# Kernel optimization log

Hardware: AMD Instinct MI355X
Metric: run time of the kernel (lower is better)

The kernel has to match this reference:

```python
import jax, jax.numpy as jnp
import numpy as np

DIM = 768
HEADS = 12
HEAD_DIM = DIM // HEADS
SCALE = HEAD_DIM ** (-0.5)


def setup_inputs() -> dict:
    key = jax.random.key(0)
    k1, k2, k3, k4 = jax.random.split(key, 4)
    B, N = 2, 48 * 48
    x = jax.random.normal(k1, (B, N, DIM), dtype=jnp.float32)
    qkv_w = jax.random.normal(k2, (3 * DIM, DIM), dtype=jnp.float32) * (DIM ** -0.5)
    proj_w = jax.random.normal(k3, (DIM, DIM), dtype=jnp.float32) * (DIM ** -0.5)
    proj_b = jax.random.normal(k4, (DIM,), dtype=jnp.float32) * 0.02
    return {"x": x, "H": 48, "W": 48, "qkv_w": qkv_w, "proj_w": proj_w, "proj_b": proj_b}


def reference(x, H, W, qkv_w, proj_w, proj_b):
    B, N, C = x.shape
    h, d = HEADS, HEAD_DIM
    # qkv linear (no bias): [B,N,3C], then split into per-head q,k,v [B,h,N,d]
    qkv = jnp.einsum('bnc,fc->bnf', x, qkv_w)
    qkv = qkv.reshape(B, N, 3, h, d).transpose(2, 0, 3, 1, 4)
    q, k, v = qkv[0], qkv[1], qkv[2]
    attn = jnp.einsum('bhnd,bhmd->bhnm', q, k) * SCALE  # [B,h,N,N]
    attn = jax.nn.softmax(attn, axis=-1)
    out = jnp.einsum('bhnm,bhmd->bhnd', attn, v)  # [B,h,N,d]
    out = out.transpose(0, 2, 1, 3).reshape(B, N, C)
    out = jnp.einsum('bnc,fc->bnf', out, proj_w) + proj_b
    return out
```

## Files before the change

kernel.cpp:

```cpp
#include <hip/hip_runtime.h>

#define B_    2
#define N_    2304
#define C_    768
#define HEADS 12
#define D_    64
#define F3    2304
#define M_    (B_*N_)
#define SPLITS 2
#define KSPAN (N_/SPLITS)
#define QSCALE 0.18033688011112042f

typedef __attribute__((ext_vector_type(8)))  short bfrag;
typedef __attribute__((ext_vector_type(4)))  float ffrag;
typedef __attribute__((ext_vector_type(16))) float ffrag16;
typedef __attribute__((ext_vector_type(4)))  unsigned ufrag;

__device__ __forceinline__ short f2bf(float f) {
    unsigned u = __float_as_uint(f);
    u += 0x7fff + ((u >> 16) & 1);
    return (short)(u >> 16);
}

__device__ __forceinline__ void gl2lds16(const void* g, void* l) {
    __builtin_amdgcn_global_load_lds(
        (const __attribute__((address_space(1))) void*)g,
        (__attribute__((address_space(3))) void*)l, 16, 0, 0);
}

__device__ __forceinline__ unsigned pktrunc(float a, float b) {
    return __builtin_amdgcn_perm(__float_as_uint(a), __float_as_uint(b),
                                 0x03020706u);
}

__global__ __launch_bounds__(256) void cast_all(const float* __restrict__ x,
                                                const float* __restrict__ qw,
                                                const float* __restrict__ pw,
                                                short* __restrict__ dst) {
    const int nx4 = (M_*C_)/4, nq4 = (F3*C_)/4, np4 = (C_*C_)/4;
    int i = blockIdx.x * 256 + threadIdx.x;
    if (i >= nx4 + nq4 + np4) return;
    const float* src; int off;
    if (i < nx4)            { src = x;  off = i; }
    else if (i < nx4 + nq4) { src = qw; off = i - nx4; }
    else                    { src = pw; off = i - nx4 - nq4; }
    float4 v = ((const float4*)src)[off];
    short4 o;
    o.x = f2bf(v.x); o.y = f2bf(v.y); o.z = f2bf(v.z); o.w = f2bf(v.w);
    ((short4*)dst)[i] = o;
}

__global__ __launch_bounds__(256) void qkv_gemm(const short* __restrict__ xb,
                                                const short* __restrict__ wb,
                                                short* __restrict__ Qb,
                                                short* __restrict__ Kb,
                                                short* __restrict__ Vtb) {
    __shared__ short As[128*64];
    __shared__ short Bs[128*64];
    const int t = threadIdx.x;
    const int w = t >> 6, lane = t & 63;
    const int quad = lane >> 4, l15 = lane & 15;
    const int wr = w >> 1, wc = w & 1;
    const int m0 = blockIdx.y * 128, f0 = blockIdx.x * 128;
    const int lrow = lane >> 3;
    const int lc   = (lane & 7) ^ lrow;
    const int r7   = l15 & 7;

    ffrag acc[4][4] = {};

    for (int k0 = 0; k0 < C_; k0 += 64) {
        __syncthreads();
        #pragma unroll
        for (int r = 0; r < 4; ++r) {
            int seg = r*4 + w;
            int row = seg*8 + lrow;
            gl2lds16(xb + (size_t)(m0+row)*C_ + k0 + lc*8, As + seg*512);
            gl2lds16(wb + (size_t)(f0+row)*C_ + k0 + lc*8, Bs + seg*512);
        }
        __syncthreads();
        #pragma unroll
        for (int s = 0; s < 2; ++s) {
            bfrag af[4], bf[4];
            int slot = (s*4 + quad) ^ r7;
            #pragma unroll
            for (int i = 0; i < 4; ++i)
                af[i] = *(const bfrag*)(As + (wr*64 + i*16 + l15)*64 + slot*8);
            #pragma unroll
            for (int j = 0; j < 4; ++j)
                bf[j] = *(const bfrag*)(Bs + (wc*64 + j*16 + l15)*64 + slot*8);
            #pragma unroll
            for (int i = 0; i < 4; ++i)
                #pragma unroll
                for (int j = 0; j < 4; ++j)
                    acc[i][j] = __builtin_amdgcn_mfma_f32_16x16x32_bf16(af[i], bf[j], acc[i][j], 0, 0, 0);
        }
    }

    const int b   = m0 / N_;
    const int seg = f0 + wc*64;
    const int which = seg / C_;
    const int head  = (seg - which*C_) >> 6;
    const int bh    = b*HEADS + head;
    const int nbase = (m0 - b*N_) + wr*64 + quad*4;

    if (which == 0) {
        #pragma unroll
        for (int i = 0; i < 4; ++i) {
            int n0 = nbase + i*16;
            #pragma unroll
            for (int j = 0; j < 4; ++j) {
                int d = j*16 + l15;
                #pragma unroll
                for (int r = 0; r < 4; ++r)
                    Qb[((size_t)bh*N_ + n0 + r)*D_ + d] = f2bf(acc[i][j][r] * QSCALE);
            }
        }
    } else if (which == 1) {
        #pragma unroll
        for (int i = 0; i < 4; ++i) {
            int n0 = nbase + i*16;
            #pragma unroll
            for (int j = 0; j < 4; ++j) {
                int d = j*16 + l15;
                #pragma unroll
                for (int r = 0; r < 4; ++r)
                    Kb[((size_t)bh*N_ + n0 + r)*D_ + d] = f2bf(acc[i][j][r]);
            }
        }
    } else {
        #pragma unroll
        for (int i = 0; i < 4; ++i) {
            int n0 = nbase + i*16;
            #pragma unroll
            for (int j = 0; j < 4; ++j) {
                int d = j*16 + l15;
                short4 vv;
                vv.x = f2bf(acc[i][j][0]);
                vv.y = f2bf(acc[i][j][1]);
                vv.z = f2bf(acc[i][j][2]);
                vv.w = f2bf(acc[i][j][3]);
                *(short4*)(Vtb + ((size_t)bh*D_ + d)*N_ + n0) = vv;
            }
        }
    }
}

__global__ __launch_bounds__(128, 3) void attn_mfma(const short* __restrict__ Qb,
                                                    const short* __restrict__ Kb,
                                                    const short* __restrict__ Vtb,
                                                    float* __restrict__ Opart,
                                                    float* __restrict__ lpart) {
    __shared__ short Ks[2][64*64];
    __shared__ short Vts[2][64*64];
    const int t = threadIdx.x;
    const int w = t >> 6, lane = t & 63;
    const int l31 = lane & 31, hi = lane >> 5;
    const int bh = blockIdx.x, q0 = blockIdx.y * 64;
    const int split = blockIdx.z;
    const int kbase = split * KSPAN;
    const size_t base = (size_t)bh * N_ * D_;
    const int lrow = lane >> 3;
    const int lc   = (lane & 7) ^ lrow;

    #pragma unroll
    for (int r = 0; r < 4; ++r) {
        int s = r*2 + w;
        int row = s*8 + lrow;
        gl2lds16(Qb + base + (size_t)(q0+row)*D_ + lc*8, Ks[0] + s*512);
    }
    __syncthreads();

    bfrag qf[4];
    {
        int row = w*32 + l31, r7 = row & 7;
        #pragma unroll
        for (int kc = 0; kc < 4; ++kc)
            qf[kc] = *(const bfrag*)(Ks[0] + row*64 + ((kc*2 + hi) ^ r7)*8);
    }

    bfrag vones;
    #pragma unroll
    for (int j = 0; j < 8; ++j) vones[j] = (short)0x3f80;

    ffrag16 oacc[2], lfr;
    #pragma unroll
    for (int r = 0; r < 16; ++r) { oacc[0][r] = 0.f; oacc[1][r] = 0.f; lfr[r] = 0.f; }

    for (int k0 = kbase; k0 < kbase + KSPAN; k0 += 128) {
        __syncthreads();
        #pragma unroll
        for (int r = 0; r < 4; ++r) {
            int s = r*2 + w;
            int row = s*8 + lrow;
            gl2lds16(Kb  + base + (size_t)(k0+row)*D_ + lc*8,         Ks[0]  + s*512);
            gl2lds16(Vtb + (size_t)(bh*D_ + row)*N_ + k0 + lc*8,      Vts[0] + s*512);
            gl2lds16(Kb  + base + (size_t)(k0+64+row)*D_ + lc*8,      Ks[1]  + s*512);
            gl2lds16(Vtb + (size_t)(bh*D_ + row)*N_ + k0 + 64 + lc*8, Vts[1] + s*512);
        }
        __syncthreads();

        #pragma unroll
        for (int tb = 0; tb < 2; ++tb) {
            ufrag pfr[4];
            #pragma unroll
            for (int kt = 0; kt < 2; ++kt) {
                ffrag16 s;
                #pragma unroll
                for (int r = 0; r < 16; ++r) s[r] = 0.f;
                int row = kt*32 + l31, r7 = row & 7;
                #pragma unroll
                for (int kc = 0; kc < 4; ++kc) {
                    bfrag kf = *(const bfrag*)(Ks[tb] + row*64 + ((kc*2 + hi) ^ r7)*8);
                    s = __builtin_amdgcn_mfma_f32_32x32x16_bf16(kf, qf[kc], s, 0, 0, 0);
                }
                #pragma unroll
                for (int r = 0; r < 16; ++r)
                    s[r] = __builtin_amdgcn_exp2f(s[r]);
                unsigned q01_0 = pktrunc(s[0],  s[1]),  q23_0 = pktrunc(s[2],  s[3]);
                unsigned q01_1 = pktrunc(s[4],  s[5]),  q23_1 = pktrunc(s[6],  s[7]);
                unsigned q01_2 = pktrunc(s[8],  s[9]),  q23_2 = pktrunc(s[10], s[11]);
                unsigned q01_3 = pktrunc(s[12], s[13]), q23_3 = pktrunc(s[14], s[15]);
                unsigned r0 = __shfl_xor(hi ? q01_0 : q01_1, 32, 64);
                unsigned r1 = __shfl_xor(hi ? q23_0 : q23_1, 32, 64);
                unsigned r2 = __shfl_xor(hi ? q01_2 : q01_3, 32, 64);
                unsigned r3 = __shfl_xor(hi ? q23_2 : q23_3, 32, 64);
                ufrag lo, hif;
                lo[0] = hi ? r0 : q01_0;  lo[1] = hi ? r1 : q23_0;
                lo[2] = hi ? q01_1 : r0;  lo[3] = hi ? q23_1 : r1;
                hif[0] = hi ? r2 : q01_2; hif[1] = hi ? r3 : q23_2;
                hif[2] = hi ? q01_3 : r2; hif[3] = hi ? q23_3 : r3;
                pfr[kt*2]     = lo;
                pfr[kt*2 + 1] = hif;
            }

            #pragma unroll
            for (int kc = 0; kc < 4; ++kc) {
                bfrag pf = __builtin_bit_cast(bfrag, pfr[kc]);
                #pragma unroll
                for (int dt = 0; dt < 2; ++dt) {
                    int row = dt*32 + l31, r7 = row & 7;
                    bfrag vf = *(const bfrag*)(Vts[tb] + row*64 + ((kc*2 + hi) ^ r7)*8);
                    oacc[dt] = __builtin_amdgcn_mfma_f32_32x32x16_bf16(pf, vf, oacc[dt], 0, 0, 0);
                }
                lfr = __builtin_amdgcn_mfma_f32_32x32x16_bf16(pf, vones, lfr, 0, 0, 0);
            }
        }
    }

    const int b = bh / HEADS, head = bh - b*HEADS;
    float* Op = Opart + (size_t)split * M_ * C_;
    float* lp = lpart + (size_t)split * (B_*HEADS) * N_;

    if (l31 == 0) {
        #pragma unroll
        for (int r = 0; r < 16; ++r) {
            int n = q0 + w*32 + (r & 3) + 8*(r >> 2) + 4*hi;
            lp[bh*N_ + n] = lfr[r];
        }
    }

    #pragma unroll
    for (int dt = 0; dt < 2; ++dt)
        #pragma unroll
        for (int r = 0; r < 16; ++r) {
            int n = q0 + w*32 + (r & 3) + 8*(r >> 2) + 4*hi;
            int c = head*D_ + dt*32 + l31;
            Op[((size_t)b*N_ + n)*C_ + c] = oacc[dt][r];
        }
}

__global__ __launch_bounds__(256) void attn_merge(const float* __restrict__ Opart,
                                                  const float* __restrict__ lpart,
                                                  short* __restrict__ Ob) {
    int i = blockIdx.x * 256 + threadIdx.x;
    int m = i / (C_/4);
    int c = (i - m*(C_/4)) * 4;
    int b = m / N_, n = m - b*N_;
    int bh = b*HEADS + (c >> 6);
    float4 o0 = ((const float4*)Opart)[i];
    float4 o1 = ((const float4*)(Opart + (size_t)M_*C_))[i];
    float l = lpart[bh*N_ + n] + lpart[(B_*HEADS)*N_ + bh*N_ + n];
    float inv = 1.f / l;
    short4 o;
    o.x = f2bf((o0.x + o1.x) * inv);
    o.y = f2bf((o0.y + o1.y) * inv);
    o.z = f2bf((o0.z + o1.z) * inv);
    o.w = f2bf((o0.w + o1.w) * inv);
    ((short4*)Ob)[i] = o;
}

__global__ __launch_bounds__(256) void proj_gemm(const short* __restrict__ Ab,
                                                 const short* __restrict__ wb,
                                                 const float* __restrict__ bias,
                                                 float* __restrict__ out) {
    __shared__ short As[128*32];
    __shared__ short Bs[128*32];
    const int t = threadIdx.x;
    const int w = t >> 6, lane = t & 63;
    const int quad = lane >> 4, l15 = lane & 15;
    const int wr = w >> 1, wc = w & 1;
    const int m0 = blockIdx.y * 128, f0 = blockIdx.x * 128;

    ffrag acc[4][4] = {};

    for (int k0 = 0; k0 < C_; k0 += 32) {
        __syncthreads();
        #pragma unroll
        for (int r = 0; r < 2; ++r) {
            int seg = r*4 + w;
            int row = seg*16 + (lane >> 2);
            int kk  = (lane & 3) * 8;
            gl2lds16(Ab + (size_t)(m0+row)*C_ + k0 + kk, As + seg*512);
            gl2lds16(wb + (size_t)(f0+row)*C_ + k0 + kk, Bs + seg*512);
        }
        __syncthreads();
        bfrag af[4], bf[4];
        #pragma unroll
        for (int i = 0; i < 4; ++i)
            af[i] = *(const bfrag*)(As + (wr*64 + i*16 + l15)*32 + quad*8);
        #pragma unroll
        for (int j = 0; j < 4; ++j)
            bf[j] = *(const bfrag*)(Bs + (wc*64 + j*16 + l15)*32 + quad*8);
        #pragma unroll
        for (int i = 0; i < 4; ++i)
            #pragma unroll
            for (int j = 0; j < 4; ++j)
                acc[i][j] = __builtin_amdgcn_mfma_f32_16x16x32_bf16(af[i], bf[j], acc[i][j], 0, 0, 0);
    }

    #pragma unroll
    for (int i = 0; i < 4; ++i) {
        int mbase = m0 + wr*64 + i*16 + quad*4;
        #pragma unroll
        for (int j = 0; j < 4; ++j) {
            int f = f0 + wc*64 + j*16 + l15;
            float bv = bias[f];
            #pragma unroll
            for (int r = 0; r < 4; ++r)
                out[(size_t)(mbase + r)*C_ + f] = acc[i][j][r] + bv;
        }
    }
}

extern "C" void kernel_launch(void* const* d_in, const int* in_sizes, int n_in,
                              void* d_out, int out_size, void* d_ws, size_t ws_size,
                              hipStream_t stream) {
    const float* x      = (const float*)d_in[0];
    const float* qkv_w  = (const float*)d_in[3];
    const float* proj_w = (const float*)d_in[4];
    const float* proj_b = (const float*)d_in[5];
    float* out = (float*)d_out;

    const size_t nx = (size_t)M_ * C_;
    const size_t nq = (size_t)F3 * C_;
    const size_t np = (size_t)C_ * C_;
    short* xb  = (short*)d_ws;
    short* qwb = xb  + nx;
    short* pwb = qwb + nq;
    short* Qb  = pwb + np;
    short* Kb  = Qb  + nx;
    short* Vtb = Kb  + nx;
    short* Ob  = Vtb + nx;
    float* Opart = (float*)(Ob + nx);
    float* lpart = Opart + (size_t)SPLITS * M_ * C_;

    const int ncast4 = (int)((nx + nq + np) / 4);
    cast_all<<<dim3((ncast4 + 255)/256), 256, 0, stream>>>(x, qkv_w, proj_w, xb);

    qkv_gemm<<<dim3(F3/128, M_/128), 256, 0, stream>>>(xb, qwb, Qb, Kb, Vtb);
    attn_mfma<<<dim3(B_*HEADS, N_/64, SPLITS), 128, 0, stream>>>(Qb, Kb, Vtb, Opart, lpart);
    attn_merge<<<dim3(((int)(nx/4) + 255)/256), 256, 0, stream>>>(Opart, lpart, Ob);
    proj_gemm<<<dim3(C_/128, M_/128), 256, 0, stream>>>(Ob, pwb, proj_b, out);
}
```

Baseline: 214.6 us.

## Double-buffer K/V tiles in attention and widen proj GEMM k-tile with swizzle

```diff
diff --git a/kernel.cpp b/kernel.cpp
--- a/kernel.cpp
+++ b/kernel.cpp
@@ -145,11 +145,11 @@
     }
 }
 
-__global__ __launch_bounds__(128, 3) void attn_mfma(const short* __restrict__ Qb,
-                                                    const short* __restrict__ Kb,
-                                                    const short* __restrict__ Vtb,
-                                                    float* __restrict__ Opart,
-                                                    float* __restrict__ lpart) {
+__global__ __launch_bounds__(128) void attn_mfma(const short* __restrict__ Qb,
+                                                 const short* __restrict__ Kb,
+                                                 const short* __restrict__ Vtb,
+                                                 float* __restrict__ Opart,
+                                                 float* __restrict__ lpart) {
     __shared__ short Ks[2][64*64];
     __shared__ short Vts[2][64*64];
     const int t = threadIdx.x;
@@ -166,7 +166,7 @@
     for (int r = 0; r < 4; ++r) {
         int s = r*2 + w;
         int row = s*8 + lrow;
-        gl2lds16(Qb + base + (size_t)(q0+row)*D_ + lc*8, Ks[0] + s*512);
+        gl2lds16(Qb + base + (size_t)(q0+row)*D_ + lc*8, Ks[1] + s*512);
     }
     __syncthreads();
 
@@ -175,8 +175,17 @@
         int row = w*32 + l31, r7 = row & 7;
         #pragma unroll
         for (int kc = 0; kc < 4; ++kc)
-            qf[kc] = *(const bfrag*)(Ks[0] + row*64 + ((kc*2 + hi) ^ r7)*8);
-    }
+            qf[kc] = *(const bfrag*)(Ks[1] + row*64 + ((kc*2 + hi) ^ r7)*8);
+    }
+
+    #pragma unroll
+    for (int r = 0; r < 4; ++r) {
+        int s = r*2 + w;
+        int row = s*8 + lrow;
+        gl2lds16(Kb  + base + (size_t)(kbase+row)*D_ + lc*8,    Ks[0]  + s*512);
+        gl2lds16(Vtb + (size_t)(bh*D_ + row)*N_ + kbase + lc*8, Vts[0] + s*512);
+    }
+    __syncthreads();
 
     bfrag vones;
     #pragma unroll
@@ -186,65 +195,66 @@
     #pragma unroll
     for (int r = 0; r < 16; ++r) { oacc[0][r] = 0.f; oacc[1][r] = 0.f; lfr[r] = 0.f; }
 
-    for (int k0 = kbase; k0 < kbase + KSPAN; k0 += 128) {
-        __syncthreads();
-        #pragma unroll
-        for (int r = 0; r < 4; ++r) {
-            int s = r*2 + w;
-            int row = s*8 + lrow;
-            gl2lds16(Kb  + base + (size_t)(k0+row)*D_ + lc*8,         Ks[0]  + s*512);
-            gl2lds16(Vtb + (size_t)(bh*D_ + row)*N_ + k0 + lc*8,      Vts[0] + s*512);
-            gl2lds16(Kb  + base + (size_t)(k0+64+row)*D_ + lc*8,      Ks[1]  + s*512);
-            gl2lds16(Vtb + (size_t)(bh*D_ + row)*N_ + k0 + 64 + lc*8, Vts[1] + s*512);
-        }
-        __syncthreads();
-
-        #pragma unroll
-        for (int tb = 0; tb < 2; ++tb) {
-            ufrag pfr[4];
-            #pragma unroll
-            for (int kt = 0; kt < 2; ++kt) {
-                ffrag16 s;
-                #pragma unroll
-                for (int r = 0; r < 16; ++r) s[r] = 0.f;
-                int row = kt*32 + l31, r7 = row & 7;
-                #pragma unroll
-                for (int kc = 0; kc < 4; ++kc) {
-                    bfrag kf = *(const bfrag*)(Ks[tb] + row*64 + ((kc*2 + hi) ^ r7)*8);
-                    s = __builtin_amdgcn_mfma_f32_32x32x16_bf16(kf, qf[kc], s, 0, 0, 0);
-                }
-                #pragma unroll
-                for (int r = 0; r < 16; ++r)
-                    s[r] = __builtin_amdgcn_exp2f(s[r]);
-                unsigned q01_0 = pktrunc(s[0],  s[1]),  q23_0 = pktrunc(s[2],  s[3]);
-                unsigned q01_1 = pktrunc(s[4],  s[5]),  q23_1 = pktrunc(s[6],  s[7]);
-                unsigned q01_2 = pktrunc(s[8],  s[9]),  q23_2 = pktrunc(s[10], s[11]);
-                unsigned q01_3 = pktrunc(s[12], s[13]), q23_3 = pktrunc(s[14], s[15]);
-                unsigned r0 = __shfl_xor(hi ? q01_0 : q01_1, 32, 64);
-                unsigned r1 = __shfl_xor(hi ? q23_0 : q23_1, 32, 64);
-                unsigned r2 = __shfl_xor(hi ? q01_2 : q01_3, 32, 64);
-                unsigned r3 = __shfl_xor(hi ? q23_2 : q23_3, 32, 64);
-                ufrag lo, hif;
-                lo[0] = hi ? r0 : q01_0;  lo[1] = hi ? r1 : q23_0;
-                lo[2] = hi ? q01_1 : r0;  lo[3] = hi ? q23_1 : r1;
-                hif[0] = hi ? r2 : q01_2; hif[1] = hi ? r3 : q23_2;
-                hif[2] = hi ? q01_3 : r2; hif[3] = hi ? q23_3 : r3;
-                pfr[kt*2]     = lo;
-                pfr[kt*2 + 1] = hif;
-            }
-
+    const int nIters = KSPAN / 64;
+    for (int it = 0; it < nIters; ++it) {
+        const int cur = it & 1, nxt = cur ^ 1;
+
+        if (it + 1 < nIters) {
+            int k1 = kbase + (it + 1) * 64;
+            #pragma unroll
+            for (int r = 0; r < 4; ++r) {
+                int s = r*2 + w;
+                int row = s*8 + lrow;
+                gl2lds16(Kb  + base + (size_t)(k1+row)*D_ + lc*8, Ks[nxt]  + s*512);
+                gl2lds16(Vtb + (size_t)(bh*D_ + row)*N_ + k1 + lc*8, Vts[nxt] + s*512);
+            }
+        }
+
+        ufrag pfr[4];
+        #pragma unroll
+        for (int kt = 0; kt < 2; ++kt) {
+            ffrag16 s;
+            #pragma unroll
+            for (int r = 0; r < 16; ++r) s[r] = 0.f;
+            int row = kt*32 + l31, r7 = row & 7;
             #pragma unroll
             for (int kc = 0; kc < 4; ++kc) {
-                bfrag pf = __builtin_bit_cast(bfrag, pfr[kc]);
-                #pragma unroll
-                for (int dt = 0; dt < 2; ++dt) {
-                    int row = dt*32 + l31, r7 = row & 7;
-                    bfrag vf = *(const bfrag*)(Vts[tb] + row*64 + ((kc*2 + hi) ^ r7)*8);
-                    oacc[dt] = __builtin_amdgcn_mfma_f32_32x32x16_bf16(pf, vf, oacc[dt], 0, 0, 0);
-                }
-                lfr = __builtin_amdgcn_mfma_f32_32x32x16_bf16(pf, vones, lfr, 0, 0, 0);
-            }
-        }
+                bfrag kf = *(const bfrag*)(Ks[cur] + row*64 + ((kc*2 + hi) ^ r7)*8);
+                s = __builtin_amdgcn_mfma_f32_32x32x16_bf16(kf, qf[kc], s, 0, 0, 0);
+            }
+            #pragma unroll
+            for (int r = 0; r < 16; ++r)
+                s[r] = __builtin_amdgcn_exp2f(s[r]);
+            unsigned q01_0 = pktrunc(s[0],  s[1]),  q23_0 = pktrunc(s[2],  s[3]);
+            unsigned q01_1 = pktrunc(s[4],  s[5]),  q23_1 = pktrunc(s[6],  s[7]);
+            unsigned q01_2 = pktrunc(s[8],  s[9]),  q23_2 = pktrunc(s[10], s[11]);
+            unsigned q01_3 = pktrunc(s[12], s[13]), q23_3 = pktrunc(s[14], s[15]);
+            unsigned r0 = __shfl_xor(hi ? q01_0 : q01_1, 32, 64);
+            unsigned r1 = __shfl_xor(hi ? q23_0 : q23_1, 32, 64);
+            unsigned r2 = __shfl_xor(hi ? q01_2 : q01_3, 32, 64);
+            unsigned r3 = __shfl_xor(hi ? q23_2 : q23_3, 32, 64);
+            ufrag lo, hif;
+            lo[0] = hi ? r0 : q01_0;  lo[1] = hi ? r1 : q23_0;
+            lo[2] = hi ? q01_1 : r0;  lo[3] = hi ? q23_1 : r1;
+            hif[0] = hi ? r2 : q01_2; hif[1] = hi ? r3 : q23_2;
+            hif[2] = hi ? q01_3 : r2; hif[3] = hi ? q23_3 : r3;
+            pfr[kt*2]     = lo;
+            pfr[kt*2 + 1] = hif;
+        }
+
+        #pragma unroll
+        for (int kc = 0; kc < 4; ++kc) {
+            bfrag pf = __builtin_bit_cast(bfrag, pfr[kc]);
+            #pragma unroll
+            for (int dt = 0; dt < 2; ++dt) {
+                int row = dt*32 + l31, r7 = row & 7;
+                bfrag vf = *(const bfrag*)(Vts[cur] + row*64 + ((kc*2 + hi) ^ r7)*8);
+                oacc[dt] = __builtin_amdgcn_mfma_f32_32x32x16_bf16(pf, vf, oacc[dt], 0, 0, 0);
+            }
+            lfr = __builtin_amdgcn_mfma_f32_32x32x16_bf16(pf, vones, lfr, 0, 0, 0);
+        }
+
+        __syncthreads();
     }
 
     const int b = bh / HEADS, head = bh - b*HEADS;
@@ -293,39 +303,45 @@
                                                  const short* __restrict__ wb,
                                                  const float* __restrict__ bias,
                                                  float* __restrict__ out) {
-    __shared__ short As[128*32];
-    __shared__ short Bs[128*32];
+    __shared__ short As[128*64];
+    __shared__ short Bs[128*64];
     const int t = threadIdx.x;
     const int w = t >> 6, lane = t & 63;
     const int quad = lane >> 4, l15 = lane & 15;
     const int wr = w >> 1, wc = w & 1;
     const int m0 = blockIdx.y * 128, f0 = blockIdx.x * 128;
+    const int lrow = lane >> 3;
+    const int lc   = (lane & 7) ^ lrow;
+    const int r7   = l15 & 7;
 
     ffrag acc[4][4] = {};
 
-    for (int k0 = 0; k0 < C_; k0 += 32) {
-        __syncthreads();
-        #pragma unroll
-        for (int r = 0; r < 2; ++r) {
+    for (int k0 = 0; k0 < C_; k0 += 64) {
+        __syncthreads();
+        #pragma unroll
+        for (int r = 0; r < 4; ++r) {
             int seg = r*4 + w;
-            int row = seg*16 + (lane >> 2);
-            int kk  = (lane & 3) * 8;
-            gl2lds16(Ab + (size_t)(m0+row)*C_ + k0 + kk, As + seg*512);
-            gl2lds16(wb + (size_t)(f0+row)*C_ + k0 + kk, Bs + seg*512);
-        }
-        __syncthreads();
-        bfrag af[4], bf[4];
-        #pragma unroll
-        for (int i = 0; i < 4; ++i)
-            af[i] = *(const bfrag*)(As + (wr*64 + i*16 + l15)*32 + quad*8);
-        #pragma unroll
-        for (int j = 0; j < 4; ++j)
-            bf[j] = *(const bfrag*)(Bs + (wc*64 + j*16 + l15)*32 + quad*8);
-        #pragma unroll
-        for (int i = 0; i < 4; ++i)
+            int row = seg*8 + lrow;
+            gl2lds16(Ab + (size_t)(m0+row)*C_ + k0 + lc*8, As + seg*512);
+            gl2lds16(wb + (size_t)(f0+row)*C_ + k0 + lc*8, Bs + seg*512);
+        }
+        __syncthreads();
+        #pragma unroll
+        for (int s = 0; s < 2; ++s) {
+            bfrag af[4], bf[4];
+            int slot = (s*4 + quad) ^ r7;
+            #pragma unroll
+            for (int i = 0; i < 4; ++i)
+                af[i] = *(const bfrag*)(As + (wr*64 + i*16 + l15)*64 + slot*8);
             #pragma unroll
             for (int j = 0; j < 4; ++j)
-                acc[i][j] = __builtin_amdgcn_mfma_f32_16x16x32_bf16(af[i], bf[j], acc[i][j], 0, 0, 0);
+                bf[j] = *(const bfrag*)(Bs + (wc*64 + j*16 + l15)*64 + slot*8);
+            #pragma unroll
+            for (int i = 0; i < 4; ++i)
+                #pragma unroll
+                for (int j = 0; j < 4; ++j)
+                    acc[i][j] = __builtin_amdgcn_mfma_f32_16x16x32_bf16(af[i], bf[j], acc[i][j], 0, 0, 0);
+        }
     }
 
     #pragma unroll
```

Result: slower. 220.7 us (+2.9%).

## Load K fragments directly from global, double-buffer V tiles, reorder grid

Applied to the files above, without the earlier changes.

```diff
diff --git a/kernel.cpp b/kernel.cpp
--- a/kernel.cpp
+++ b/kernel.cpp
@@ -145,17 +145,16 @@
     }
 }
 
-__global__ __launch_bounds__(128, 3) void attn_mfma(const short* __restrict__ Qb,
-                                                    const short* __restrict__ Kb,
-                                                    const short* __restrict__ Vtb,
-                                                    float* __restrict__ Opart,
-                                                    float* __restrict__ lpart) {
-    __shared__ short Ks[2][64*64];
+__global__ __launch_bounds__(128) void attn_mfma(const short* __restrict__ Qb,
+                                                 const short* __restrict__ Kb,
+                                                 const short* __restrict__ Vtb,
+                                                 float* __restrict__ Opart,
+                                                 float* __restrict__ lpart) {
     __shared__ short Vts[2][64*64];
     const int t = threadIdx.x;
     const int w = t >> 6, lane = t & 63;
     const int l31 = lane & 31, hi = lane >> 5;
-    const int bh = blockIdx.x, q0 = blockIdx.y * 64;
+    const int q0 = blockIdx.x * 64, bh = blockIdx.y;
     const int split = blockIdx.z;
     const int kbase = split * KSPAN;
     const size_t base = (size_t)bh * N_ * D_;
@@ -166,7 +165,7 @@
     for (int r = 0; r < 4; ++r) {
         int s = r*2 + w;
         int row = s*8 + lrow;
-        gl2lds16(Qb + base + (size_t)(q0+row)*D_ + lc*8, Ks[0] + s*512);
+        gl2lds16(Qb + base + (size_t)(q0+row)*D_ + lc*8, Vts[0] + s*512);
     }
     __syncthreads();
 
@@ -175,7 +174,15 @@
         int row = w*32 + l31, r7 = row & 7;
         #pragma unroll
         for (int kc = 0; kc < 4; ++kc)
-            qf[kc] = *(const bfrag*)(Ks[0] + row*64 + ((kc*2 + hi) ^ r7)*8);
+            qf[kc] = *(const bfrag*)(Vts[0] + row*64 + ((kc*2 + hi) ^ r7)*8);
+    }
+    __syncthreads();
+
+    #pragma unroll
+    for (int r = 0; r < 4; ++r) {
+        int s = r*2 + w;
+        int row = s*8 + lrow;
+        gl2lds16(Vtb + (size_t)(bh*D_ + row)*N_ + kbase + lc*8, Vts[0] + s*512);
     }
 
     bfrag vones;
@@ -186,64 +193,68 @@
     #pragma unroll
     for (int r = 0; r < 16; ++r) { oacc[0][r] = 0.f; oacc[1][r] = 0.f; lfr[r] = 0.f; }
 
-    for (int k0 = kbase; k0 < kbase + KSPAN; k0 += 128) {
-        __syncthreads();
-        #pragma unroll
-        for (int r = 0; r < 4; ++r) {
-            int s = r*2 + w;
-            int row = s*8 + lrow;
-            gl2lds16(Kb  + base + (size_t)(k0+row)*D_ + lc*8,         Ks[0]  + s*512);
-            gl2lds16(Vtb + (size_t)(bh*D_ + row)*N_ + k0 + lc*8,      Vts[0] + s*512);
-            gl2lds16(Kb  + base + (size_t)(k0+64+row)*D_ + lc*8,      Ks[1]  + s*512);
-            gl2lds16(Vtb + (size_t)(bh*D_ + row)*N_ + k0 + 64 + lc*8, Vts[1] + s*512);
-        }
-        __syncthreads();
-
-        #pragma unroll
-        for (int tb = 0; tb < 2; ++tb) {
-            ufrag pfr[4];
-            #pragma unroll
-            for (int kt = 0; kt < 2; ++kt) {
-                ffrag16 s;
-                #pragma unroll
-                for (int r = 0; r < 16; ++r) s[r] = 0.f;
-                int row = kt*32 + l31, r7 = row & 7;
-                #pragma unroll
-                for (int kc = 0; kc < 4; ++kc) {
-                    bfrag kf = *(const bfrag*)(Ks[tb] + row*64 + ((kc*2 + hi) ^ r7)*8);
-                    s = __builtin_amdgcn_mfma_f32_32x32x16_bf16(kf, qf[kc], s, 0, 0, 0);
-                }
-                #pragma unroll
-                for (int r = 0; r < 16; ++r)
-                    s[r] = __builtin_amdgcn_exp2f(s[r]);
-                unsigned q01_0 = pktrunc(s[0],  s[1]),  q23_0 = pktrunc(s[2],  s[3]);
-                unsigned q01_1 = pktrunc(s[4],  s[5]),  q23_1 = pktrunc(s[6],  s[7]);
-                unsigned q01_2 = pktrunc(s[8],  s[9]),  q23_2 = pktrunc(s[10], s[11]);
-                unsigned q01_3 = pktrunc(s[12], s[13]), q23_3 = pktrunc(s[14], s[15]);
-                unsigned r0 = __shfl_xor(hi ? q01_0 : q01_1, 32, 64);
-                unsigned r1 = __shfl_xor(hi ? q23_0 : q23_1, 32, 64);
-                unsigned r2 = __shfl_xor(hi ? q01_2 : q01_3, 32, 64);
-                unsigned r3 = __shfl_xor(hi ? q23_2 : q23_3, 32, 64);
-                ufrag lo, hif;
-                lo[0] = hi ? r0 : q01_0;  lo[1] = hi ? r1 : q23_0;
-                lo[2] = hi ? q01_1 : r0;  lo[3] = hi ? q23_1 : r1;
-                hif[0] = hi ? r2 : q01_2; hif[1] = hi ? r3 : q23_2;
-                hif[2] = hi ? q01_3 : r2; hif[3] = hi ? q23_3 : r3;
-                pfr[kt*2]     = lo;
-                pfr[kt*2 + 1] = hif;
-            }
-
-            #pragma unroll
-            for (int kc = 0; kc < 4; ++kc) {
-                bfrag pf = __builtin_bit_cast(bfrag, pfr[kc]);
-                #pragma unroll
-                for (int dt = 0; dt < 2; ++dt) {
-                    int row = dt*32 + l31, r7 = row & 7;
-                    bfrag vf = *(const bfrag*)(Vts[tb] + row*64 + ((kc*2 + hi) ^ r7)*8);
-                    oacc[dt] = __builtin_amdgcn_mfma_f32_32x32x16_bf16(pf, vf, oacc[dt], 0, 0, 0);
-                }
-                lfr = __builtin_amdgcn_mfma_f32_32x32x16_bf16(pf, vones, lfr, 0, 0, 0);
-            }
+    const int nIters = KSPAN / 64;
+    for (int it = 0; it < nIters; ++it) {
+        const int cur = it & 1, nxt = cur ^ 1;
+        const int k0  = kbase + it * 64;
+
+        __syncthreads();
+
+        if (it + 1 < nIters) {
+            int k1 = k0 + 64;
+            #pragma unroll
+            for (int r = 0; r < 4; ++r) {
+                int s = r*2 + w;
+                int row = s*8 + lrow;
+                gl2lds16(Vtb + (size_t)(bh*D_ + row)*N_ + k1 + lc*8, Vts[nxt] + s*512);
+            }
+        }
+
+        ufrag pfr[4];
+        #pragma unroll
+        for (int kt = 0; kt < 2; ++kt) {
+            const short* kp = Kb + base + (size_t)(k0 + kt*32 + l31)*D_ + hi*8;
+            bfrag kf0 = *(const bfrag*)(kp);
+            bfrag kf1 = *(const bfrag*)(kp + 16);
+            bfrag kf2 = *(const bfrag*)(kp + 32);
+            bfrag kf3 = *(const bfrag*)(kp + 48);
+            ffrag16 s;
+            #pragma unroll
+            for (int r = 0; r < 16; ++r) s[r] = 0.f;
+            s = __builtin_amdgcn_mfma_f32_32x32x16_bf16(kf0, qf[0], s, 0, 0, 0);
+            s = __builtin_amdgcn_mfma_f32_32x32x16_bf16(kf1, qf[1], s, 0, 0, 0);
+            s = __builtin_amdgcn_mfma_f32_32x32x16_bf16(kf2, qf[2], s, 0, 0, 0);
+            s = __builtin_amdgcn_mfma_f32_32x32x16_bf16(kf3, qf[3], s, 0, 0, 0);
+            #pragma unroll
+            for (int r = 0; r < 16; ++r)
+                s[r] = __builtin_amdgcn_exp2f(s[r]);
+            unsigned q01_0 = pktrunc(s[0],  s[1]),  q23_0 = pktrunc(s[2],  s[3]);
+            unsigned q01_1 = pktrunc(s[4],  s[5]),  q23_1 = pktrunc(s[6],  s[7]);
+            unsigned q01_2 = pktrunc(s[8],  s[9]),  q23_2 = pktrunc(s[10], s[11]);
+            unsigned q01_3 = pktrunc(s[12], s[13]), q23_3 = pktrunc(s[14], s[15]);
+            unsigned r0 = __shfl_xor(hi ? q01_0 : q01_1, 32, 64);
+            unsigned r1 = __shfl_xor(hi ? q23_0 : q23_1, 32, 64);
+            unsigned r2 = __shfl_xor(hi ? q01_2 : q01_3, 32, 64);
+            unsigned r3 = __shfl_xor(hi ? q23_2 : q23_3, 32, 64);
+            ufrag lo, hif;
+            lo[0] = hi ? r0 : q01_0;  lo[1] = hi ? r1 : q23_0;
+            lo[2] = hi ? q01_1 : r0;  lo[3] = hi ? q23_1 : r1;
+            hif[0] = hi ? r2 : q01_2; hif[1] = hi ? r3 : q23_2;
+            hif[2] = hi ? q01_3 : r2; hif[3] = hi ? q23_3 : r3;
+            pfr[kt*2]     = lo;
+            pfr[kt*2 + 1] = hif;
+        }
+
+        #pragma unroll
+        for (int kc = 0; kc < 4; ++kc) {
+            bfrag pf = __builtin_bit_cast(bfrag, pfr[kc]);
+            #pragma unroll
+            for (int dt = 0; dt < 2; ++dt) {
+                int row = dt*32 + l31, r7 = row & 7;
+                bfrag vf = *(const bfrag*)(Vts[cur] + row*64 + ((kc*2 + hi) ^ r7)*8);
+                oacc[dt] = __builtin_amdgcn_mfma_f32_32x32x16_bf16(pf, vf, oacc[dt], 0, 0, 0);
+            }
+            lfr = __builtin_amdgcn_mfma_f32_32x32x16_bf16(pf, vones, lfr, 0, 0, 0);
         }
     }
 
@@ -368,7 +379,7 @@
     cast_all<<<dim3((ncast4 + 255)/256), 256, 0, stream>>>(x, qkv_w, proj_w, xb);
 
     qkv_gemm<<<dim3(F3/128, M_/128), 256, 0, stream>>>(xb, qwb, Qb, Kb, Vtb);
-    attn_mfma<<<dim3(B_*HEADS, N_/64, SPLITS), 128, 0, stream>>>(Qb, Kb, Vtb, Opart, lpart);
+    attn_mfma<<<dim3(N_/64, B_*HEADS, SPLITS), 128, 0, stream>>>(Qb, Kb, Vtb, Opart, lpart);
     attn_merge<<<dim3(((int)(nx/4) + 255)/256), 256, 0, stream>>>(Opart, lpart, Ob);
     proj_gemm<<<dim3(C_/128, M_/128), 256, 0, stream>>>(Ob, pwb, proj_b, out);
 }
```

After: 241.1 us. 1.12x slower.
